# Kernel optimization log

Hardware: AMD Instinct MI355X
Metric: run time of the kernel (lower is better)

## Reference

```python
import jax, jax.numpy as jnp
import numpy as np

B, T = 1024, 8192
NUM_WORDS = 2048  # ph2word.max() + 1, forced by construction in setup_inputs
OFFSET = 1.0
LAMBDA_P, LAMBDA_W, LAMBDA_S = 0.6, 0.3, 0.1
RULES_SCALE = 0.3
INIT_TOKENS = np.array([94, 122, 100, 92, 43, 27], dtype=np.int32)
INIT_DURS = np.array([2.0, 3.0, 2.0, 2.0, 5.0, 5.0], dtype=np.float32)
RATIO_TOKENS = np.array([44, 28, 29, 27, 121, 43], dtype=np.int32)


def setup_inputs() -> dict:
    key = jax.random.key(0)
    k1, k2, k3, k4 = jax.random.split(key, 4)
    dur_pred = jax.random.uniform(k1, (B, T), dtype=jnp.float32) * 10.0
    dur_gt = jax.random.uniform(k2, (B, T), dtype=jnp.float32) * 10.0
    ph2word = jnp.sort(jax.random.randint(k3, (B, T), 0, NUM_WORDS, dtype=jnp.int32), axis=1)
    ph2word = ph2word.at[:, -1].set(NUM_WORDS - 1)  # guarantee max == NUM_WORDS-1 (static shape)
    txt_tokens = jax.random.randint(k4, (B, T), 0, 150, dtype=jnp.int32)
    return {"dur_pred": dur_pred, "dur_gt": dur_gt, "ph2word": ph2word, "txt_tokens": txt_tokens}


def _linear2log(x):
    return jnp.log(x + OFFSET)


def _mse(a, b):
    d = a - b
    return jnp.mean(d * d)


def _dur_rules(dur_pred, txt_tokens):
    # Vectorized form of the sequential double loop. At step i the carry value
    # dur_rules[:, i] is unconditionally reset to dur_pred[:, i], so the ratio
    # rule's forward write to i+1 never survives; final value is
    #   dur_pred[i] - self_adjust(i) + neighbor_gaps_from(i+1).
    tok = txt_tokens[..., None]  # [B,T,1]
    in_init = jnp.any(tok == jnp.asarray(INIT_TOKENS), axis=-1)
    expected = jnp.sum(jnp.where(tok == jnp.asarray(INIT_TOKENS), jnp.asarray(INIT_DURS), 0.0), axis=-1)
    gap1 = dur_pred - expected
    fire1 = in_init & (gap1 > 0)
    gap1 = jnp.where(fire1, gap1, 0.0)

    in_ratio = jnp.any(tok == jnp.asarray(RATIO_TOKENS), axis=-1)
    dp_next = jnp.concatenate([dur_pred[:, 1:], jnp.zeros_like(dur_pred[:, :1])], axis=1)
    valid_next = jnp.arange(dur_pred.shape[1]) < dur_pred.shape[1] - 1
    fire2 = in_ratio & valid_next[None, :] & (3.0 * dur_pred > dp_next)
    gap2 = jnp.where(fire2, dur_pred - dp_next / 3.0, 0.0)

    # ratio rule overwrites (not adds to) the self position when it fires
    self_adj = jnp.where(fire2, gap2, jnp.where(fire1, gap1, 0.0))
    dur_rules = dur_pred - self_adj
    # gaps from iteration i+1 are added to position i (only for i+1 >= 1, always true)
    dur_rules = dur_rules.at[:, :-1].add((gap1 + gap2)[:, 1:])
    return dur_rules


def reference(dur_pred, dur_gt, ph2word, txt_tokens):
    dur_gt = dur_gt.astype(dur_pred.dtype)

    dur_rules = _dur_rules(dur_pred, txt_tokens)
    rules_loss = RULES_SCALE * _mse(_linear2log(dur_pred), _linear2log(dur_rules))

    pdur_loss = LAMBDA_P * _mse(_linear2log(dur_pred), _linear2log(dur_gt))

    dp_c = jnp.maximum(dur_pred, 0.0)
    seg = lambda d, s: jax.ops.segment_sum(d, s, num_segments=NUM_WORDS)
    wdur_pred = jax.vmap(seg)(dp_c, ph2word)[:, 1:]
    wdur_gt = jax.vmap(seg)(dur_gt, ph2word)[:, 1:]
    wdur_loss = LAMBDA_W * _mse(_linear2log(wdur_pred), _linear2log(wdur_gt))

    sdur_pred = jnp.sum(dp_c, axis=1)
    sdur_gt = jnp.sum(dur_gt, axis=1)
    sdur_loss = LAMBDA_S * _mse(_linear2log(sdur_pred), _linear2log(sdur_gt))

    return pdur_loss + wdur_loss + sdur_loss + rules_loss
```

## Files before the change

kernel.cpp:

```cpp
#include <hip/hip_runtime.h>

constexpr int Bn  = 1024;
constexpr int Tn  = 8192;
constexpr int Wn  = 2048;
constexpr int TPB = 512;
constexpr int BPR = 4;
constexpr int SEG = Tn / BPR;

__device__ __forceinline__ void rule_eval(float dp, float dpn, int tok, bool valid_next,
                                          float& g1, float& g2, float& sa) {
  float expected;
  bool in_init = true;
  switch (tok) {
    case 94:  expected = 2.f; break;
    case 122: expected = 3.f; break;
    case 100: expected = 2.f; break;
    case 92:  expected = 2.f; break;
    case 43:  expected = 5.f; break;
    case 27:  expected = 5.f; break;
    default:  expected = 0.f; in_init = false; break;
  }
  float t1 = dp - expected;
  bool fire1 = in_init && (t1 > 0.f);
  g1 = fire1 ? t1 : 0.f;
  bool in_ratio = (tok == 44) | (tok == 28) | (tok == 29) |
                  (tok == 27) | (tok == 121) | (tok == 43);
  bool fire2 = in_ratio && valid_next && (3.f * dp > dpn);
  g2 = fire2 ? (dp - dpn * (1.f / 3.f)) : 0.f;
  sa = fire2 ? g2 : (fire1 ? g1 : 0.f);
}

__device__ __forceinline__ float wave_reduce(float v) {
  #pragma unroll
  for (int o = 32; o > 0; o >>= 1) v += __shfl_down(v, o, 64);
  return v;
}

__global__ __launch_bounds__(TPB, 8) void loss_kernel(
    const float* __restrict__ dur_pred, const float* __restrict__ dur_gt,
    const int* __restrict__ ph2word, const int* __restrict__ txt,
    float4* __restrict__ partials)
{
  __shared__ float wp[Wn];
  __shared__ float wg[Wn];
  __shared__ float sacc[5];
  __shared__ int   smeta[3];

  const int row = blockIdx.x >> 2;
  const int sub = blockIdx.x & 3;
  const int s = sub * SEG;
  const int e = s + SEG;
  const size_t roff = (size_t)row * Tn;
  const float* __restrict__ dpr = dur_pred + roff;
  const float* __restrict__ dgr = dur_gt + roff;
  const int*   __restrict__ pwr = ph2word + roff;
  const int*   __restrict__ tkr = txt + roff;

  const int tid  = threadIdx.x;
  const int lane = tid & 63;
  const bool is63 = (lane == 63);
  const int base = s + tid * 4;

  float4 dp4 = *reinterpret_cast<const float4*>(dpr + base);
  float4 dg4 = *reinterpret_cast<const float4*>(dgr + base);
  int4   pw4 = *reinterpret_cast<const int4*>(pwr + base);
  int4   tk4 = *reinterpret_cast<const int4*>(tkr + base);

  float nb_dp = 0.f, nb_dp1 = 0.f; int nb_tk = -1;
  if (is63) {
    const int p = base + 4;
    if (p < Tn) { nb_dp = dpr[p]; nb_dp1 = dpr[p + 1]; nb_tk = tkr[p]; }
  }

  if (tid == 0) {
    int lo;
    if (s == 0) lo = 1;
    else {
      const int pw_prev = pwr[s - 1];
      lo = (pw_prev == pw4.x) ? pw4.x + 1 : pw4.x;
      if (lo < 1) lo = 1;
    }
    smeta[0] = lo;
    smeta[1] = (e < Tn) ? pwr[e] : -1;
  }
  if (tid == TPB - 1) smeta[2] = pw4.w;

  {
    const float4 z = {0.f, 0.f, 0.f, 0.f};
    *reinterpret_cast<float4*>(&wp[tid * 4]) = z;
    *reinterpret_cast<float4*>(&wg[tid * 4]) = z;
  }
  if (tid < 5) sacc[tid] = 0.f;
  __syncthreads();

  float g1v[4], g2v[4], sav[4];
  rule_eval(dp4.x, dp4.y, tk4.x, true, g1v[0], g2v[0], sav[0]);
  rule_eval(dp4.y, dp4.z, tk4.y, true, g1v[1], g2v[1], sav[1]);
  rule_eval(dp4.z, dp4.w, tk4.z, true, g1v[2], g2v[2], sav[2]);
  float gg0 = g1v[0] + g2v[0];

  float dpn3 = __shfl_down(dp4.x, 1, 64);
  float ggn  = __shfl_down(gg0,  1, 64);
  {
    float ng1, ng2, nsa_;
    rule_eval(nb_dp, nb_dp1, nb_tk, base + 4 < Tn - 1, ng1, ng2, nsa_);
    dpn3 = is63 ? nb_dp : dpn3;
    ggn  = is63 ? (ng1 + ng2) : ggn;
  }
  rule_eval(dp4.w, dpn3, tk4.w, base + 3 < Tn - 1, g1v[3], g2v[3], sav[3]);

  float dpx[4] = {dp4.x, dp4.y, dp4.z, dp4.w};
  float dgl[4] = {dg4.x, dg4.y, dg4.z, dg4.w};
  float addv[4] = {g1v[1] + g2v[1], g1v[2] + g2v[2], g1v[3] + g2v[3],
                   (base + 3 < Tn - 1) ? ggn : 0.f};

  float pdur_s = 0.f, rules_s = 0.f, sp = 0.f, sg = 0.f;
  #pragma unroll
  for (int j = 0; j < 4; ++j) {
    float dp = dpx[j];
    float dr = dp - sav[j] + addv[j];
    float lp = __logf(dp + 1.f);
    float dlr = lp - __logf(dr + 1.f);
    rules_s += dlr * dlr;
    float dlg = lp - __logf(dgl[j] + 1.f);
    pdur_s += dlg * dlg;
    sp += fmaxf(dp, 0.f);
    sg += dgl[j];
  }

  {
    int pwl[4] = {pw4.x, pw4.y, pw4.z, pw4.w};
    int curw = pwl[0];
    float ap = 0.f, ag = 0.f;
    #pragma unroll
    for (int j = 0; j < 4; ++j) {
      if (pwl[j] != curw) {
        atomicAdd(&wp[curw], ap);
        atomicAdd(&wg[curw], ag);
        curw = pwl[j]; ap = 0.f; ag = 0.f;
      }
      ap += fmaxf(dpx[j], 0.f);
      ag += dgl[j];
    }
    atomicAdd(&wp[curw], ap);
    atomicAdd(&wg[curw], ag);
  }

  __syncthreads();

  const int lo        = smeta[0];
  const int pw_next   = smeta[1];
  const int pw_lastm1 = smeta[2];
  const int hi = (e == Tn) ? Wn : ((pw_lastm1 == pw_next) ? pw_next + 1 : pw_next);

  if (tid < 64) {
    const int w_end = pw_lastm1;
    const bool doscan = (e < Tn) && (pw_next == w_end) && (w_end >= lo);
    if (doscan) {
      float ap = 0.f, ag = 0.f;
      int p = e + lane;
      for (;;) {
        bool in = (p < Tn) && (pwr[p] == w_end);
        if (in) { float d = dpr[p]; ap += fmaxf(d, 0.f); ag += dgr[p]; }
        if (__ballot(in) != ~0ull) break;
        p += 64;
      }
      ap = wave_reduce(ap);
      ag = wave_reduce(ag);
      if (lane == 0) { atomicAdd(&wp[w_end], ap); atomicAdd(&wg[w_end], ag); }
    }
  }
  __syncthreads();

  float wd_s = 0.f;
  for (int w = lo + tid; w < hi; w += TPB) {
    float d = __logf(wp[w] + 1.f) - __logf(wg[w] + 1.f);
    wd_s += d * d;
  }

  pdur_s  = wave_reduce(pdur_s);
  rules_s = wave_reduce(rules_s);
  sp      = wave_reduce(sp);
  sg      = wave_reduce(sg);
  wd_s    = wave_reduce(wd_s);
  if (lane == 0) {
    atomicAdd(&sacc[0], pdur_s);
    atomicAdd(&sacc[1], rules_s);
    atomicAdd(&sacc[2], sp);
    atomicAdd(&sacc[3], sg);
    atomicAdd(&sacc[4], wd_s);
  }
  __syncthreads();

  if (tid == 0) {
    float4 a; a.x = sacc[0]; a.y = sacc[1]; a.z = sacc[4]; a.w = sacc[2];
    float4 b; b.x = sacc[3]; b.y = 0.f; b.z = 0.f; b.w = 0.f;
    partials[(size_t)blockIdx.x * 2]     = a;
    partials[(size_t)blockIdx.x * 2 + 1] = b;
  }
}

__global__ __launch_bounds__(1024) void finalize_kernel(
    const float4* __restrict__ partials, float* __restrict__ out)
{
  __shared__ double wsum[16];
  const int r = threadIdx.x;
  double pd = 0.0, rl = 0.0, wd = 0.0;
  float sp = 0.f, sg = 0.f;
  #pragma unroll
  for (int j = 0; j < BPR; ++j) {
    const size_t idx = ((size_t)r * BPR + j) * 2;
    float4 a = partials[idx];
    float4 b = partials[idx + 1];
    pd += (double)a.x; rl += (double)a.y; wd += (double)a.z;
    sp += a.w; sg += b.x;
  }
  float ds = __logf(sp + 1.f) - __logf(sg + 1.f);
  double contrib = 0.6 * pd / ((double)Bn * (double)Tn)
                 + 0.3 * rl / ((double)Bn * (double)Tn)
                 + 0.3 * wd / ((double)Bn * (double)(Wn - 1))
                 + 0.1 * (double)(ds * ds) / (double)Bn;
  #pragma unroll
  for (int o = 32; o > 0; o >>= 1) contrib += __shfl_down(contrib, o, 64);
  if ((threadIdx.x & 63) == 0) wsum[threadIdx.x >> 6] = contrib;
  __syncthreads();
  if (threadIdx.x == 0) {
    double t = 0.0;
    #pragma unroll
    for (int i = 0; i < 16; ++i) t += wsum[i];
    out[0] = (float)t;
  }
}

extern "C" void kernel_launch(void* const* d_in, const int* in_sizes, int n_in,
                              void* d_out, int out_size, void* d_ws, size_t ws_size,
                              hipStream_t stream) {
  const float* dur_pred = (const float*)d_in[0];
  const float* dur_gt   = (const float*)d_in[1];
  const int*   ph2word  = (const int*)d_in[2];
  const int*   txt      = (const int*)d_in[3];

  float4* partials = (float4*)d_ws;

  loss_kernel<<<Bn * BPR, TPB, 0, stream>>>(dur_pred, dur_gt, ph2word, txt, partials);
  finalize_kernel<<<1, 1024, 0, stream>>>(partials, (float*)d_out);
}
```

Before: 183.0 us.

## Defer boundary-word sums to finalize instead of scanning across block segments

Each block now writes the partial sums for its first and last word segment into the partials buffer. The finalize kernel merges boundary words across the four sub-blocks of a row and adds their log-MSE terms. This removes the extra global-memory scan of the next segment and one block-wide barrier from the main kernel. It adds a third float4 per block and some serial merge logic in finalize. Interior word handling also changes, since empty words between segments are covered only by lo/hi ranges, and the word-0 exclusion relies on curid > 0.

Result: no change. 181.1 us (-1.0%).

```diff
diff --git a/kernel.cpp b/kernel.cpp
--- a/kernel.cpp
+++ b/kernel.cpp
@@ -44,12 +44,11 @@
   __shared__ float wp[Wn];
   __shared__ float wg[Wn];
   __shared__ float sacc[5];
-  __shared__ int   smeta[3];
+  __shared__ int   smeta[2];
 
   const int row = blockIdx.x >> 2;
   const int sub = blockIdx.x & 3;
   const int s = sub * SEG;
-  const int e = s + SEG;
   const size_t roff = (size_t)row * Tn;
   const float* __restrict__ dpr = dur_pred + roff;
   const float* __restrict__ dgr = dur_gt + roff;
@@ -72,18 +71,8 @@
     if (p < Tn) { nb_dp = dpr[p]; nb_dp1 = dpr[p + 1]; nb_tk = tkr[p]; }
   }
 
-  if (tid == 0) {
-    int lo;
-    if (s == 0) lo = 1;
-    else {
-      const int pw_prev = pwr[s - 1];
-      lo = (pw_prev == pw4.x) ? pw4.x + 1 : pw4.x;
-      if (lo < 1) lo = 1;
-    }
-    smeta[0] = lo;
-    smeta[1] = (e < Tn) ? pwr[e] : -1;
-  }
-  if (tid == TPB - 1) smeta[2] = pw4.w;
+  if (tid == 0)       smeta[0] = pw4.x;
+  if (tid == TPB - 1) smeta[1] = pw4.w;
 
   {
     const float4 z = {0.f, 0.f, 0.f, 0.f};
@@ -148,32 +137,11 @@
 
   __syncthreads();
 
-  const int lo        = smeta[0];
-  const int pw_next   = smeta[1];
-  const int pw_lastm1 = smeta[2];
-  const int hi = (e == Tn) ? Wn : ((pw_lastm1 == pw_next) ? pw_next + 1 : pw_next);
-
-  if (tid < 64) {
-    const int w_end = pw_lastm1;
-    const bool doscan = (e < Tn) && (pw_next == w_end) && (w_end >= lo);
-    if (doscan) {
-      float ap = 0.f, ag = 0.f;
-      int p = e + lane;
-      for (;;) {
-        bool in = (p < Tn) && (pwr[p] == w_end);
-        if (in) { float d = dpr[p]; ap += fmaxf(d, 0.f); ag += dgr[p]; }
-        if (__ballot(in) != ~0ull) break;
-        p += 64;
-      }
-      ap = wave_reduce(ap);
-      ag = wave_reduce(ag);
-      if (lane == 0) { atomicAdd(&wp[w_end], ap); atomicAdd(&wg[w_end], ag); }
-    }
-  }
-  __syncthreads();
+  const int wf = smeta[0];
+  const int wl = smeta[1];
 
   float wd_s = 0.f;
-  for (int w = lo + tid; w < hi; w += TPB) {
+  for (int w = wf + 1 + tid; w < wl; w += TPB) {
     float d = __logf(wp[w] + 1.f) - __logf(wg[w] + 1.f);
     wd_s += d * d;
   }
@@ -193,10 +161,16 @@
   __syncthreads();
 
   if (tid == 0) {
-    float4 a; a.x = sacc[0]; a.y = sacc[1]; a.z = sacc[4]; a.w = sacc[2];
-    float4 b; b.x = sacc[3]; b.y = 0.f; b.z = 0.f; b.w = 0.f;
-    partials[(size_t)blockIdx.x * 2]     = a;
-    partials[(size_t)blockIdx.x * 2 + 1] = b;
+    float4 a, b, c;
+    a.x = sacc[0]; a.y = sacc[1]; a.z = sacc[4]; a.w = sacc[2];
+    b.x = sacc[3];
+    if (wf != wl) { b.y = wp[wf]; b.z = wg[wf]; b.w = __int_as_float(wf); }
+    else          { b.y = 0.f;    b.z = 0.f;    b.w = __int_as_float(-1); }
+    c.x = wp[wl]; c.y = wg[wl]; c.z = __int_as_float(wl); c.w = 0.f;
+    const size_t idx = (size_t)blockIdx.x * 3;
+    partials[idx]     = a;
+    partials[idx + 1] = b;
+    partials[idx + 2] = c;
   }
 }
 
@@ -207,19 +181,41 @@
   const int r = threadIdx.x;
   double pd = 0.0, rl = 0.0, wd = 0.0;
   float sp = 0.f, sg = 0.f;
+  int curid = -1; float cp = 0.f, cg = 0.f;
+
   #pragma unroll
   for (int j = 0; j < BPR; ++j) {
-    const size_t idx = ((size_t)r * BPR + j) * 2;
+    const size_t idx = ((size_t)r * BPR + j) * 3;
     float4 a = partials[idx];
     float4 b = partials[idx + 1];
+    float4 c = partials[idx + 2];
     pd += (double)a.x; rl += (double)a.y; wd += (double)a.z;
     sp += a.w; sg += b.x;
-  }
+    const int wfi = __float_as_int(b.w);
+    const int wla = __float_as_int(c.z);
+    if (wfi >= 0) {
+      if (wfi != curid) {
+        if (curid > 0) { float d = __logf(cp + 1.f) - __logf(cg + 1.f); wd += (double)(d * d); }
+        curid = wfi; cp = 0.f; cg = 0.f;
+      }
+      cp += b.y; cg += b.z;
+    }
+    if (wla >= 0) {
+      if (wla != curid) {
+        if (curid > 0) { float d = __logf(cp + 1.f) - __logf(cg + 1.f); wd += (double)(d * d); }
+        curid = wla; cp = 0.f; cg = 0.f;
+      }
+      cp += c.x; cg += c.y;
+    }
+  }
+  if (curid > 0) { float d = __logf(cp + 1.f) - __logf(cg + 1.f); wd += (double)(d * d); }
+
   float ds = __logf(sp + 1.f) - __logf(sg + 1.f);
   double contrib = 0.6 * pd / ((double)Bn * (double)Tn)
                  + 0.3 * rl / ((double)Bn * (double)Tn)
                  + 0.3 * wd / ((double)Bn * (double)(Wn - 1))
                  + 0.1 * (double)(ds * ds) / (double)Bn;
+
   #pragma unroll
   for (int o = 32; o > 0; o >>= 1) contrib += __shfl_down(contrib, o, 64);
   if ((threadIdx.x & 63) == 0) wsum[threadIdx.x >> 6] = contrib;
```
